# Kernel tuning notes

Hardware: AMD Instinct MI355X
Metric: run time of the kernel (lower is better)

Reference implementation:

```python
import jax, jax.numpy as jnp
import numpy as np

WS = 7          # window size
SHIFT = 3       # shift size for mask pattern
HP = WP = 224   # padded feature-map size -> (224/7)^2 = 1024 windows
DIM = 128
HEADS = 4
BATCH_IMGS = 8


def _rel_pos_index(ws: int) -> np.ndarray:
    coords = np.stack(np.meshgrid(np.arange(ws), np.arange(ws), indexing='ij'))  # [2,ws,ws]
    cf = coords.reshape(2, -1)                              # [2, ws*ws]
    rel = cf[:, :, None] - cf[:, None, :]                   # [2, N, N]
    rel = rel.transpose(1, 2, 0).copy()                     # [N, N, 2]
    rel[:, :, 0] += ws - 1
    rel[:, :, 1] += ws - 1
    rel[:, :, 0] *= 2 * ws - 1
    return rel.sum(-1).astype(np.int32)                     # [N, N]


def _shift_mask(Hp: int, Wp: int, ws: int, shift: int) -> np.ndarray:
    img = np.zeros((Hp, Wp), dtype=np.float32)
    slices = (slice(0, -ws), slice(-ws, -shift), slice(-shift, None))
    cnt = 0
    for hs in slices:
        for wsl in slices:
            img[hs, wsl] = cnt
            cnt += 1
    # window partition -> [nW, ws*ws]
    mw = img.reshape(Hp // ws, ws, Wp // ws, ws).transpose(0, 2, 1, 3).reshape(-1, ws * ws)
    am = mw[:, None, :] - mw[:, :, None]                    # [nW, N, N]
    return np.where(am != 0, np.float32(-100.0), np.float32(0.0))


def setup_inputs() -> dict:
    key = jax.random.key(0)
    ks = jax.random.split(key, 6)
    nW = (HP // WS) * (WP // WS)                            # 1024
    B_ = BATCH_IMGS * nW                                    # 8192
    N = WS * WS                                             # 49
    x = jax.random.normal(ks[0], (B_, N, DIM), dtype=jnp.float32)
    qkv_w = jax.random.normal(ks[1], (3 * DIM, DIM), dtype=jnp.float32) * (DIM ** -0.5)
    qkv_b = jax.random.normal(ks[2], (3 * DIM,), dtype=jnp.float32) * 0.02
    proj_w = jax.random.normal(ks[3], (DIM, DIM), dtype=jnp.float32) * (DIM ** -0.5)
    proj_b = jax.random.normal(ks[4], (DIM,), dtype=jnp.float32) * 0.02
    rpb_table = jax.random.normal(ks[5], ((2 * WS - 1) ** 2, HEADS), dtype=jnp.float32) * 0.02
    mask = jnp.asarray(_shift_mask(HP, WP, WS, SHIFT))      # [1024, 49, 49]
    rel_index = jnp.asarray(_rel_pos_index(WS))             # [49, 49] int32
    return {"x": x, "qkv_w": qkv_w, "qkv_b": qkv_b, "proj_w": proj_w,
            "proj_b": proj_b, "rpb_table": rpb_table, "mask": mask,
            "rel_index": rel_index}


def reference(x, qkv_w, qkv_b, proj_w, proj_b, rpb_table, mask, rel_index):
    B_, N, C = x.shape
    H = HEADS
    hd = C // H
    scale = hd ** -0.5
    qkv = x @ qkv_w.T + qkv_b                               # [B_, N, 3C]
    qkv = qkv.reshape(B_, N, 3, H, hd).transpose(2, 0, 3, 1, 4)  # [3, B_, H, N, hd]
    q, k, v = qkv[0], qkv[1], qkv[2]
    attn = jnp.einsum('bhnd,bhmd->bhnm', q * scale, k)      # [B_, H, N, N]
    # gathered relative position bias: table[(N*N)] -> [N, N, H] -> [H, N, N]
    bias = rpb_table[rel_index.reshape(-1)].reshape(N, N, H).transpose(2, 0, 1)
    attn = attn + bias[None]
    nW = mask.shape[0]
    attn = attn.reshape(B_ // nW, nW, H, N, N) + mask[None, :, None]
    attn = attn.reshape(B_, H, N, N)
    attn = jax.nn.softmax(attn, axis=-1)
    out = jnp.einsum('bhnm,bhmd->bhnd', attn, v)            # [B_, H, N, hd]
    out = out.transpose(0, 2, 1, 3).reshape(B_, N, C)
    return out @ proj_w.T + proj_b
```

## Files before the change

### kernel.cpp

```cpp
#include <hip/hip_runtime.h>

typedef __bf16 bf16;
typedef bf16 bf16x4 __attribute__((ext_vector_type(4)));
typedef bf16 bf16x8 __attribute__((ext_vector_type(8)));
typedef float f32x4 __attribute__((ext_vector_type(4)));

#define MFMA16(a, b, c) __builtin_amdgcn_mfma_f32_16x16x32_bf16((a), (b), (c), 0, 0, 0)

#define XS_OFF 0
#define QF_OFF 13328
#define PAF_OFF 0
#define KF_OFF 32768
#define VTF_OFF 49152
#define AO_OFF 32768
#define SMEM_BYTES 65536

__global__ void prep_kernel(const float* __restrict__ qkv_w, const float* __restrict__ proj_w,
                            const float* __restrict__ rpb, const int* __restrict__ rel,
                            bf16* __restrict__ wq, bf16* __restrict__ wp,
                            float* __restrict__ biasg) {
  int i = blockIdx.x * 256 + threadIdx.x;
  if (i < 49152) {
    wq[i] = (bf16)qkv_w[i];
  } else if (i < 65536) {
    wp[i - 49152] = (bf16)proj_w[i - 49152];
  } else if (i < 75140) {
    int t = i - 65536;
    int nm = t % 2401, h = t / 2401;
    biasg[t] = rpb[rel[nm] * 4 + h];
  }
}

__global__ void __launch_bounds__(256, 2)
swin_kernel(const float* __restrict__ x, const float* __restrict__ qkv_b,
            const float* __restrict__ proj_b, const float* __restrict__ maskp,
            const bf16* __restrict__ wq, const bf16* __restrict__ wp,
            const float* __restrict__ biasg, float* __restrict__ outp) {
  __shared__ __align__(16) unsigned char smem[SMEM_BYTES];
  bf16* xsL  = (bf16*)(smem + XS_OFF);
  bf16* qfL  = (bf16*)(smem + QF_OFF);
  bf16* pafL = (bf16*)(smem + PAF_OFF);
  bf16* kfL  = (bf16*)(smem + KF_OFF);
  bf16* vtfL = (bf16*)(smem + VTF_OFF);
  bf16* aoL  = (bf16*)(smem + AO_OFF);

  const int tid = threadIdx.x;
  const int bi = blockIdx.x;
  const int img = bi & 7;
  const int widx = bi >> 3;
  const int b = img * 1024 + widx;
  const int w = tid >> 6;
  const int l = tid & 63;
  const int lane16 = l & 15;
  const int grp = l >> 4;
  const float scale = 0.17677669529663687f;

  {
    const float4* xb = (const float4*)(x + (size_t)b * 6272);
#pragma unroll
    for (int it = 0; it < 7; ++it) {
      int i = tid + it * 256;
      if (i < 1568) {
        float4 v = xb[i];
        int e = i << 2, row = e >> 7, col = e & 127;
        bf16x4 bv;
        bv[0] = (bf16)v.x; bv[1] = (bf16)v.y; bv[2] = (bf16)v.z; bv[3] = (bf16)v.w;
        *(bf16x4*)(xsL + row * 136 + col) = bv;
      }
    }
    int region = tid >> 5;
    int off = (tid & 31) * 8;
    bf16x8 zz;
#pragma unroll
    for (int q = 0; q < 8; ++q) zz[q] = (bf16)0.f;
    *(bf16x8*)(vtfL + (region * 2 + 1) * 512 + 256 + off) = zz;
  }
  __syncthreads();

  {
    bf16x8 ax[4][4];
#pragma unroll
    for (int nt = 0; nt < 4; ++nt) {
      int rw = nt * 16 + lane16; if (rw > 48) rw = 48;
#pragma unroll
      for (int kb = 0; kb < 4; ++kb)
        ax[nt][kb] = *(const bf16x8*)(xsL + rw * 136 + kb * 32 + grp * 8);
    }
#pragma unroll
    for (int jj = 0; jj < 6; ++jj) {
      const int jb = w * 6 + jj;
      const int j = jb * 16 + lane16;
      bf16x8 bw[4];
#pragma unroll
      for (int kb = 0; kb < 4; ++kb)
        bw[kb] = *(const bf16x8*)(wq + j * 128 + kb * 32 + grp * 8);
      const float bj = qkv_b[j];
      const int part = jb >> 3;
      const int h = (jb >> 1) & 3;
      const int d0 = (jb & 1) * 16;
#pragma unroll
      for (int nt = 0; nt < 4; ++nt) {
        f32x4 acc = {0.f, 0.f, 0.f, 0.f};
#pragma unroll
        for (int kb = 0; kb < 4; ++kb) acc = MFMA16(ax[nt][kb], bw[kb], acc);
#pragma unroll
        for (int r = 0; r < 4; ++r) {
          const int nrow = nt * 16 + grp * 4 + r;
          if (nrow < 49) {
            float v = acc[r] + bj;
            const int d = d0 + lane16;
            if (part == 0) {
              v *= scale;
              qfL[(((h * 4 + nt) * 64) + (grp * 4 + r) + ((d >> 3) << 4)) * 8 + (d & 7)] = (bf16)v;
            } else if (part == 1) {
              kfL[(((h * 4 + nt) * 64) + (grp * 4 + r) + ((d >> 3) << 4)) * 8 + (d & 7)] = (bf16)v;
            } else {
              const int dt = d >> 4, kb2 = nrow >> 5;
              const int lp = (d & 15) + (((nrow >> 3) & 3) << 4);
              vtfL[((((h * 2 + dt) * 2 + kb2) * 64) + lp) * 8 + (nrow & 7)] = (bf16)v;
            }
          }
        }
      }
    }
  }
  __syncthreads();

  const int h = w;
  f32x4 S[4][4];
  {
    bf16x8 qa[4], ka[4];
#pragma unroll
    for (int t = 0; t < 4; ++t) {
      qa[t] = *(const bf16x8*)(qfL + ((h * 4 + t) * 64 + l) * 8);
      ka[t] = *(const bf16x8*)(kfL + ((h * 4 + t) * 64 + l) * 8);
    }
#pragma unroll
    for (int nt = 0; nt < 4; ++nt)
#pragma unroll
      for (int mt = 0; mt < 4; ++mt) {
        f32x4 zz = {0.f, 0.f, 0.f, 0.f};
        S[nt][mt] = MFMA16(qa[nt], ka[mt], zz);
      }
  }
  __syncthreads();

  float rinv[4][4];
  {
    const float* biash = biasg + h * 2401;
    const float* maskw = maskp + (size_t)widx * 2401;
#pragma unroll
    for (int nt = 0; nt < 4; ++nt) {
#pragma unroll
      for (int mt = 0; mt < 4; ++mt) {
        const int m = mt * 16 + lane16;
#pragma unroll
        for (int r = 0; r < 4; ++r) {
          const int n = nt * 16 + grp * 4 + r;
          float s = S[nt][mt][r];
          if (m < 49) {
            if (n < 49) s += biash[n * 49 + m] + maskw[n * 49 + m];
          } else {
            s = -1e30f;
          }
          S[nt][mt][r] = s;
        }
      }
#pragma unroll
      for (int r = 0; r < 4; ++r) {
        float mx = fmaxf(fmaxf(S[nt][0][r], S[nt][1][r]), fmaxf(S[nt][2][r], S[nt][3][r]));
        mx = fmaxf(mx, __shfl_xor(mx, 1));
        mx = fmaxf(mx, __shfl_xor(mx, 2));
        mx = fmaxf(mx, __shfl_xor(mx, 4));
        mx = fmaxf(mx, __shfl_xor(mx, 8));
        float sum = 0.f;
#pragma unroll
        for (int mt = 0; mt < 4; ++mt) {
          float p = __expf(S[nt][mt][r] - mx);
          S[nt][mt][r] = p;
          sum += p;
        }
        sum += __shfl_xor(sum, 1);
        sum += __shfl_xor(sum, 2);
        sum += __shfl_xor(sum, 4);
        sum += __shfl_xor(sum, 8);
        rinv[nt][r] = 1.f / sum;
      }
#pragma unroll
      for (int mt = 0; mt < 4; ++mt) {
        const int m = mt * 16 + lane16;
        const int kb2 = m >> 5;
        const int lpb = (grp * 4) + (((m >> 3) & 3) << 4);
#pragma unroll
        for (int r = 0; r < 4; ++r) {
          float p = (m < 49) ? S[nt][mt][r] : 0.f;
          pafL[((((w * 4 + nt) * 2 + kb2) * 64) + lpb + r) * 8 + (m & 7)] = (bf16)p;
        }
      }
    }
  }

  {
    bf16x8 vb2[2][2], pa[4][2];
#pragma unroll
    for (int dt = 0; dt < 2; ++dt)
#pragma unroll
      for (int kb = 0; kb < 2; ++kb)
        vb2[dt][kb] = *(const bf16x8*)(vtfL + (((h * 2 + dt) * 2 + kb) * 64 + l) * 8);
#pragma unroll
    for (int nt = 0; nt < 4; ++nt)
#pragma unroll
      for (int kb = 0; kb < 2; ++kb)
        pa[nt][kb] = *(const bf16x8*)(pafL + (((w * 4 + nt) * 2 + kb) * 64 + l) * 8);
    f32x4 O[4][2];
#pragma unroll
    for (int nt = 0; nt < 4; ++nt)
#pragma unroll
      for (int dt = 0; dt < 2; ++dt) {
        f32x4 acc = {0.f, 0.f, 0.f, 0.f};
        acc = MFMA16(pa[nt][0], vb2[dt][0], acc);
        acc = MFMA16(pa[nt][1], vb2[dt][1], acc);
        O[nt][dt] = acc;
      }
    __syncthreads();
#pragma unroll
    for (int nt = 0; nt < 4; ++nt)
#pragma unroll
      for (int r = 0; r < 4; ++r) {
        const int n = nt * 16 + grp * 4 + r;
        if (n < 49) {
          const float ri = rinv[nt][r];
#pragma unroll
          for (int dt = 0; dt < 2; ++dt) {
            const int c = h * 32 + dt * 16 + lane16;
            aoL[n * 136 + c] = (bf16)(O[nt][dt][r] * ri);
          }
        }
      }
  }
  __syncthreads();

  {
    bf16x8 aa[4][4];
#pragma unroll
    for (int nt = 0; nt < 4; ++nt) {
      int rw = nt * 16 + lane16; if (rw > 48) rw = 48;
#pragma unroll
      for (int kb = 0; kb < 4; ++kb)
        aa[nt][kb] = *(const bf16x8*)(aoL + rw * 136 + kb * 32 + grp * 8);
    }
    float* outb = outp + (size_t)b * 6272;
#pragma unroll
    for (int ee = 0; ee < 2; ++ee) {
      const int eb = w * 2 + ee;
      const int e = eb * 16 + lane16;
      bf16x8 bw[4];
#pragma unroll
      for (int kb = 0; kb < 4; ++kb)
        bw[kb] = *(const bf16x8*)(wp + e * 128 + kb * 32 + grp * 8);
      const float be = proj_b[e];
#pragma unroll
      for (int nt = 0; nt < 4; ++nt) {
        f32x4 acc = {0.f, 0.f, 0.f, 0.f};
#pragma unroll
        for (int kb = 0; kb < 4; ++kb) acc = MFMA16(aa[nt][kb], bw[kb], acc);
#pragma unroll
        for (int r = 0; r < 4; ++r) {
          const int n = nt * 16 + grp * 4 + r;
          if (n < 49) outb[n * 128 + e] = acc[r] + be;
        }
      }
    }
  }
}

extern "C" void kernel_launch(void* const* d_in, const int* in_sizes, int n_in,
                              void* d_out, int out_size, void* d_ws, size_t ws_size,
                              hipStream_t stream) {
  const float* x      = (const float*)d_in[0];
  const float* qkv_w  = (const float*)d_in[1];
  const float* qkv_b  = (const float*)d_in[2];
  const float* proj_w = (const float*)d_in[3];
  const float* proj_b = (const float*)d_in[4];
  const float* rpb    = (const float*)d_in[5];
  const float* maskp  = (const float*)d_in[6];
  const int*   rel    = (const int*)d_in[7];

  bf16* wq = (bf16*)d_ws;
  bf16* wp = wq + 49152;
  float* biasg = (float*)((char*)d_ws + 131072);

  prep_kernel<<<294, 256, 0, stream>>>(qkv_w, proj_w, rpb, rel, wq, wp, biasg);
  swin_kernel<<<8192, 256, 0, stream>>>(x, qkv_b, proj_b, maskp, wq, wp, biasg,
                                        (float*)d_out);
}
```

Measured before the change: 635.3 us.

## Restructure Swin attention kernel: register-loaded x, row-major LDS layouts, padded bf16 mask

The x tile is now loaded from global memory straight into MFMA operand registers, which drops the LDS staging step and a barrier. Q, K and V^T move to padded row-major LDS layouts written with vector stores, using swapped MFMA operands. Softmax now runs row-wise in registers with vector loads of a 64x64 padded bias and a bf16 mask that the prep kernel builds on each call, and P is normalized before the PV product. LDS use drops so that three blocks fit per CU, and the output is written with float4 stores. In exchange, the prep kernel does more work per call converting the full mask, and the mask and P values are held in bf16.

```diff
diff --git a/kernel.cpp b/kernel.cpp
--- a/kernel.cpp
+++ b/kernel.cpp
@@ -7,42 +7,46 @@
 
 #define MFMA16(a, b, c) __builtin_amdgcn_mfma_f32_16x16x32_bf16((a), (b), (c), 0, 0, 0)
 
-#define XS_OFF 0
-#define QF_OFF 13328
-#define PAF_OFF 0
-#define KF_OFF 32768
-#define VTF_OFF 49152
-#define AO_OFF 32768
-#define SMEM_BYTES 65536
+#define VT_OFF 0
+#define Q_OFF 18432
+#define K_OFF 35840
+#define PN_OFF 18432
+#define AO_OFF 18432
+#define SMEM_BYTES 53248
 
 __global__ void prep_kernel(const float* __restrict__ qkv_w, const float* __restrict__ proj_w,
                             const float* __restrict__ rpb, const int* __restrict__ rel,
+                            const float* __restrict__ mask,
                             bf16* __restrict__ wq, bf16* __restrict__ wp,
-                            float* __restrict__ biasg) {
+                            float* __restrict__ biasp, bf16* __restrict__ maskb) {
   int i = blockIdx.x * 256 + threadIdx.x;
-  if (i < 49152) {
-    wq[i] = (bf16)qkv_w[i];
-  } else if (i < 65536) {
-    wp[i - 49152] = (bf16)proj_w[i - 49152];
-  } else if (i < 75140) {
-    int t = i - 65536;
-    int nm = t % 2401, h = t / 2401;
-    biasg[t] = rpb[rel[nm] * 4 + h];
+  if (i < 49152) { wq[i] = (bf16)qkv_w[i]; return; }
+  i -= 49152;
+  if (i < 16384) { wp[i] = (bf16)proj_w[i]; return; }
+  i -= 16384;
+  if (i < 16384) {
+    int h = i >> 12, n = (i >> 6) & 63, m = i & 63;
+    biasp[i] = (n < 49 && m < 49) ? rpb[rel[n * 49 + m] * 4 + h] : 0.f;
+    return;
+  }
+  i -= 16384;
+  if (i < 4194304) {
+    int wi = i >> 12, n = (i >> 6) & 63, m = i & 63;
+    maskb[i] = (bf16)((n < 49 && m < 49) ? mask[wi * 2401 + n * 49 + m] : 0.f);
   }
 }
 
-__global__ void __launch_bounds__(256, 2)
+__global__ void __launch_bounds__(256, 3)
 swin_kernel(const float* __restrict__ x, const float* __restrict__ qkv_b,
-            const float* __restrict__ proj_b, const float* __restrict__ maskp,
-            const bf16* __restrict__ wq, const bf16* __restrict__ wp,
-            const float* __restrict__ biasg, float* __restrict__ outp) {
+            const float* __restrict__ proj_b, const bf16* __restrict__ wq,
+            const bf16* __restrict__ wp, const float* __restrict__ biasp,
+            const bf16* __restrict__ maskb, float* __restrict__ outp) {
   __shared__ __align__(16) unsigned char smem[SMEM_BYTES];
-  bf16* xsL  = (bf16*)(smem + XS_OFF);
-  bf16* qfL  = (bf16*)(smem + QF_OFF);
-  bf16* pafL = (bf16*)(smem + PAF_OFF);
-  bf16* kfL  = (bf16*)(smem + KF_OFF);
-  bf16* vtfL = (bf16*)(smem + VTF_OFF);
-  bf16* aoL  = (bf16*)(smem + AO_OFF);
+  bf16* vtL = (bf16*)(smem + VT_OFF);
+  bf16* qL  = (bf16*)(smem + Q_OFF);
+  bf16* kL  = (bf16*)(smem + K_OFF);
+  bf16* pnL = (bf16*)(smem + PN_OFF);
+  bf16* aoL = (bf16*)(smem + AO_OFF);
 
   const int tid = threadIdx.x;
   const int bi = blockIdx.x;
@@ -51,76 +55,67 @@
   const int b = img * 1024 + widx;
   const int w = tid >> 6;
   const int l = tid & 63;
-  const int lane16 = l & 15;
+  const int l16 = l & 15;
   const int grp = l >> 4;
   const float scale = 0.17677669529663687f;
 
-  {
-    const float4* xb = (const float4*)(x + (size_t)b * 6272);
-#pragma unroll
-    for (int it = 0; it < 7; ++it) {
-      int i = tid + it * 256;
-      if (i < 1568) {
-        float4 v = xb[i];
-        int e = i << 2, row = e >> 7, col = e & 127;
-        bf16x4 bv;
-        bv[0] = (bf16)v.x; bv[1] = (bf16)v.y; bv[2] = (bf16)v.z; bv[3] = (bf16)v.w;
-        *(bf16x4*)(xsL + row * 136 + col) = bv;
-      }
-    }
-    int region = tid >> 5;
-    int off = (tid & 31) * 8;
-    bf16x8 zz;
-#pragma unroll
-    for (int q = 0; q < 8; ++q) zz[q] = (bf16)0.f;
-    *(bf16x8*)(vtfL + (region * 2 + 1) * 512 + 256 + off) = zz;
-  }
-  __syncthreads();
-
-  {
-    bf16x8 ax[4][4];
+  bf16x8 xf[4][4];
+  {
+    const float* xb = x + (size_t)b * 6272;
 #pragma unroll
     for (int nt = 0; nt < 4; ++nt) {
-      int rw = nt * 16 + lane16; if (rw > 48) rw = 48;
-#pragma unroll
-      for (int kb = 0; kb < 4; ++kb)
-        ax[nt][kb] = *(const bf16x8*)(xsL + rw * 136 + kb * 32 + grp * 8);
-    }
-#pragma unroll
-    for (int jj = 0; jj < 6; ++jj) {
-      const int jb = w * 6 + jj;
-      const int j = jb * 16 + lane16;
-      bf16x8 bw[4];
-#pragma unroll
-      for (int kb = 0; kb < 4; ++kb)
-        bw[kb] = *(const bf16x8*)(wq + j * 128 + kb * 32 + grp * 8);
-      const float bj = qkv_b[j];
-      const int part = jb >> 3;
-      const int h = (jb >> 1) & 3;
-      const int d0 = (jb & 1) * 16;
-#pragma unroll
-      for (int nt = 0; nt < 4; ++nt) {
-        f32x4 acc = {0.f, 0.f, 0.f, 0.f};
-#pragma unroll
-        for (int kb = 0; kb < 4; ++kb) acc = MFMA16(ax[nt][kb], bw[kb], acc);
+      int n = nt * 16 + l16; if (n > 48) n = 48;
+      const float* rp = xb + n * 128 + grp * 8;
+#pragma unroll
+      for (int kb = 0; kb < 4; ++kb) {
+        float4 lo = *(const float4*)(rp + kb * 32);
+        float4 hi = *(const float4*)(rp + kb * 32 + 4);
+        bf16x8 r;
+        r[0] = (bf16)lo.x; r[1] = (bf16)lo.y; r[2] = (bf16)lo.z; r[3] = (bf16)lo.w;
+        r[4] = (bf16)hi.x; r[5] = (bf16)hi.y; r[6] = (bf16)hi.z; r[7] = (bf16)hi.w;
+        xf[nt][kb] = r;
+      }
+    }
+  }
+#pragma unroll
+  for (int jj = 0; jj < 6; ++jj) {
+    const int jb = w * 6 + jj;
+    bf16x8 wf[4];
+    const bf16* wrow = wq + (jb * 16 + l16) * 128 + grp * 8;
+#pragma unroll
+    for (int kb = 0; kb < 4; ++kb) wf[kb] = *(const bf16x8*)(wrow + kb * 32);
+    if (jb < 16) {
+      float4 b4 = *(const float4*)(qkv_b + jb * 16 + (grp << 2));
+      const int col = ((jb & 7) << 4) + (grp << 2);
+      bf16* dst = (jb < 8) ? qL : kL;
+      const float sc = (jb < 8) ? scale : 1.f;
+#pragma unroll
+      for (int nt = 0; nt < 4; ++nt) {
+        f32x4 acc = {0.f, 0.f, 0.f, 0.f};
+#pragma unroll
+        for (int kb = 0; kb < 4; ++kb) acc = MFMA16(wf[kb], xf[nt][kb], acc);
+        bf16x4 pv;
+#pragma unroll
+        for (int r = 0; r < 4; ++r) pv[r] = (bf16)((acc[r] + b4[r]) * sc);
+        *(bf16x4*)(dst + (nt * 16 + l16) * 136 + col) = pv;
+      }
+    } else {
+      const float bj = qkv_b[jb * 16 + l16];
+      const int d = ((jb - 16) << 4) + l16;
+#pragma unroll
+      for (int nt = 0; nt < 4; ++nt) {
+        f32x4 acc = {0.f, 0.f, 0.f, 0.f};
+#pragma unroll
+        for (int kb = 0; kb < 4; ++kb) acc = MFMA16(xf[nt][kb], wf[kb], acc);
+        const int n0 = nt * 16 + (grp << 2);
+        bf16x4 pv;
 #pragma unroll
         for (int r = 0; r < 4; ++r) {
-          const int nrow = nt * 16 + grp * 4 + r;
-          if (nrow < 49) {
-            float v = acc[r] + bj;
-            const int d = d0 + lane16;
-            if (part == 0) {
-              v *= scale;
-              qfL[(((h * 4 + nt) * 64) + (grp * 4 + r) + ((d >> 3) << 4)) * 8 + (d & 7)] = (bf16)v;
-            } else if (part == 1) {
-              kfL[(((h * 4 + nt) * 64) + (grp * 4 + r) + ((d >> 3) << 4)) * 8 + (d & 7)] = (bf16)v;
-            } else {
-              const int dt = d >> 4, kb2 = nrow >> 5;
-              const int lp = (d & 15) + (((nrow >> 3) & 3) << 4);
-              vtfL[((((h * 2 + dt) * 2 + kb2) * 64) + lp) * 8 + (nrow & 7)] = (bf16)v;
-            }
-          }
-        }
+          float v = acc[r] + bj;
+          if (nt == 3) v = (n0 + r < 49) ? v : 0.f;
+          pv[r] = (bf16)v;
+        }
+        *(bf16x4*)(vtL + d * 72 + n0) = pv;
       }
     }
   }
@@ -132,142 +127,130 @@
     bf16x8 qa[4], ka[4];
 #pragma unroll
     for (int t = 0; t < 4; ++t) {
-      qa[t] = *(const bf16x8*)(qfL + ((h * 4 + t) * 64 + l) * 8);
-      ka[t] = *(const bf16x8*)(kfL + ((h * 4 + t) * 64 + l) * 8);
-    }
+      qa[t] = *(const bf16x8*)(qL + (t * 16 + l16) * 136 + h * 32 + grp * 8);
+      ka[t] = *(const bf16x8*)(kL + (t * 16 + l16) * 136 + h * 32 + grp * 8);
+    }
+#pragma unroll
+    for (int mt = 0; mt < 4; ++mt)
+#pragma unroll
+      for (int nt = 0; nt < 4; ++nt) {
+        f32x4 z = {0.f, 0.f, 0.f, 0.f};
+        S[mt][nt] = MFMA16(ka[mt], qa[nt], z);
+      }
+  }
+  __syncthreads();
+
+  {
+    const float* bh = biasp + h * 4096;
+    const bf16* mw = maskb + (size_t)widx * 4096;
+#pragma unroll
+    for (int nt = 0; nt < 4; ++nt) {
+      const int n = nt * 16 + l16;
+      const int rowo = n * 64 + (grp << 2);
+      float p[4][4];
+#pragma unroll
+      for (int mt = 0; mt < 4; ++mt) {
+        float4 b4 = *(const float4*)(bh + rowo + mt * 16);
+        bf16x4 m4 = *(const bf16x4*)(mw + rowo + mt * 16);
+#pragma unroll
+        for (int r = 0; r < 4; ++r) {
+          float s = S[mt][nt][r] + b4[r] + (float)m4[r];
+          if (mt == 3) s = ((grp << 2) + r < 1) ? s : -1e30f;
+          p[mt][r] = s;
+        }
+      }
+      float mx = p[0][0];
+#pragma unroll
+      for (int mt = 0; mt < 4; ++mt)
+#pragma unroll
+        for (int r = 0; r < 4; ++r) mx = fmaxf(mx, p[mt][r]);
+      mx = fmaxf(mx, __shfl_xor(mx, 16));
+      mx = fmaxf(mx, __shfl_xor(mx, 32));
+      float sum = 0.f;
+#pragma unroll
+      for (int mt = 0; mt < 4; ++mt)
+#pragma unroll
+        for (int r = 0; r < 4; ++r) { float e = __expf(p[mt][r] - mx); p[mt][r] = e; sum += e; }
+      sum += __shfl_xor(sum, 16);
+      sum += __shfl_xor(sum, 32);
+      const float ri = 1.f / sum;
+      if (n < 49) {
+        bf16* pd = pnL + h * 3528 + n * 72 + (grp << 2);
+#pragma unroll
+        for (int mt = 0; mt < 4; ++mt) {
+          bf16x4 pv;
+#pragma unroll
+          for (int r = 0; r < 4; ++r) pv[r] = (bf16)(p[mt][r] * ri);
+          *(bf16x4*)(pd + mt * 16) = pv;
+        }
+      }
+    }
+  }
+
+  f32x4 O[4][2];
+  {
+    bf16x8 pa[4][2], vb[2][2];
 #pragma unroll
     for (int nt = 0; nt < 4; ++nt)
 #pragma unroll
-      for (int mt = 0; mt < 4; ++mt) {
-        f32x4 zz = {0.f, 0.f, 0.f, 0.f};
-        S[nt][mt] = MFMA16(qa[nt], ka[mt], zz);
-      }
-  }
-  __syncthreads();
-
-  float rinv[4][4];
-  {
-    const float* biash = biasg + h * 2401;
-    const float* maskw = maskp + (size_t)widx * 2401;
-#pragma unroll
-    for (int nt = 0; nt < 4; ++nt) {
-#pragma unroll
-      for (int mt = 0; mt < 4; ++mt) {
-        const int m = mt * 16 + lane16;
-#pragma unroll
-        for (int r = 0; r < 4; ++r) {
-          const int n = nt * 16 + grp * 4 + r;
-          float s = S[nt][mt][r];
-          if (m < 49) {
-            if (n < 49) s += biash[n * 49 + m] + maskw[n * 49 + m];
-          } else {
-            s = -1e30f;
-          }
-          S[nt][mt][r] = s;
-        }
-      }
+      for (int kb = 0; kb < 2; ++kb)
+        pa[nt][kb] = *(const bf16x8*)(pnL + h * 3528 + (nt * 16 + l16) * 72 + kb * 32 + grp * 8);
+#pragma unroll
+    for (int dt = 0; dt < 2; ++dt)
+#pragma unroll
+      for (int kb = 0; kb < 2; ++kb)
+        vb[dt][kb] = *(const bf16x8*)(vtL + (h * 32 + dt * 16 + l16) * 72 + kb * 32 + grp * 8);
+#pragma unroll
+    for (int nt = 0; nt < 4; ++nt)
+#pragma unroll
+      for (int dt = 0; dt < 2; ++dt) {
+        f32x4 acc = {0.f, 0.f, 0.f, 0.f};
+        acc = MFMA16(pa[nt][0], vb[dt][0], acc);
+        acc = MFMA16(pa[nt][1], vb[dt][1], acc);
+        O[nt][dt] = acc;
+      }
+  }
+  __syncthreads();
+#pragma unroll
+  for (int nt = 0; nt < 4; ++nt)
+#pragma unroll
+    for (int dt = 0; dt < 2; ++dt) {
+      const int c = h * 32 + dt * 16 + l16;
 #pragma unroll
       for (int r = 0; r < 4; ++r) {
-        float mx = fmaxf(fmaxf(S[nt][0][r], S[nt][1][r]), fmaxf(S[nt][2][r], S[nt][3][r]));
-        mx = fmaxf(mx, __shfl_xor(mx, 1));
-        mx = fmaxf(mx, __shfl_xor(mx, 2));
-        mx = fmaxf(mx, __shfl_xor(mx, 4));
-        mx = fmaxf(mx, __shfl_xor(mx, 8));
-        float sum = 0.f;
-#pragma unroll
-        for (int mt = 0; mt < 4; ++mt) {
-          float p = __expf(S[nt][mt][r] - mx);
-          S[nt][mt][r] = p;
-          sum += p;
-        }
-        sum += __shfl_xor(sum, 1);
-        sum += __shfl_xor(sum, 2);
-        sum += __shfl_xor(sum, 4);
-        sum += __shfl_xor(sum, 8);
-        rinv[nt][r] = 1.f / sum;
-      }
-#pragma unroll
-      for (int mt = 0; mt < 4; ++mt) {
-        const int m = mt * 16 + lane16;
-        const int kb2 = m >> 5;
-        const int lpb = (grp * 4) + (((m >> 3) & 3) << 4);
-#pragma unroll
-        for (int r = 0; r < 4; ++r) {
-          float p = (m < 49) ? S[nt][mt][r] : 0.f;
-          pafL[((((w * 4 + nt) * 2 + kb2) * 64) + lpb + r) * 8 + (m & 7)] = (bf16)p;
-        }
-      }
-    }
-  }
-
-  {
-    bf16x8 vb2[2][2], pa[4][2];
-#pragma unroll
-    for (int dt = 0; dt < 2; ++dt)
-#pragma unroll
-      for (int kb = 0; kb < 2; ++kb)
-        vb2[dt][kb] = *(const bf16x8*)(vtfL + (((h * 2 + dt) * 2 + kb) * 64 + l) * 8);
+        const int n = nt * 16 + (grp << 2) + r;
+        aoL[n * 136 + c] = (bf16)O[nt][dt][r];
+      }
+    }
+  __syncthreads();
+
+  {
+    bf16x8 af[4][4];
 #pragma unroll
     for (int nt = 0; nt < 4; ++nt)
 #pragma unroll
-      for (int kb = 0; kb < 2; ++kb)
-        pa[nt][kb] = *(const bf16x8*)(pafL + (((w * 4 + nt) * 2 + kb) * 64 + l) * 8);
-    f32x4 O[4][2];
-#pragma unroll
-    for (int nt = 0; nt < 4; ++nt)
-#pragma unroll
-      for (int dt = 0; dt < 2; ++dt) {
-        f32x4 acc = {0.f, 0.f, 0.f, 0.f};
-        acc = MFMA16(pa[nt][0], vb2[dt][0], acc);
-        acc = MFMA16(pa[nt][1], vb2[dt][1], acc);
-        O[nt][dt] = acc;
-      }
-    __syncthreads();
-#pragma unroll
-    for (int nt = 0; nt < 4; ++nt)
-#pragma unroll
-      for (int r = 0; r < 4; ++r) {
-        const int n = nt * 16 + grp * 4 + r;
-        if (n < 49) {
-          const float ri = rinv[nt][r];
-#pragma unroll
-          for (int dt = 0; dt < 2; ++dt) {
-            const int c = h * 32 + dt * 16 + lane16;
-            aoL[n * 136 + c] = (bf16)(O[nt][dt][r] * ri);
-          }
-        }
-      }
-  }
-  __syncthreads();
-
-  {
-    bf16x8 aa[4][4];
-#pragma unroll
-    for (int nt = 0; nt < 4; ++nt) {
-      int rw = nt * 16 + lane16; if (rw > 48) rw = 48;
-#pragma unroll
       for (int kb = 0; kb < 4; ++kb)
-        aa[nt][kb] = *(const bf16x8*)(aoL + rw * 136 + kb * 32 + grp * 8);
-    }
-    float* outb = outp + (size_t)b * 6272;
+        af[nt][kb] = *(const bf16x8*)(aoL + (nt * 16 + l16) * 136 + kb * 32 + grp * 8);
+    float* ob = outp + (size_t)b * 6272;
 #pragma unroll
     for (int ee = 0; ee < 2; ++ee) {
       const int eb = w * 2 + ee;
-      const int e = eb * 16 + lane16;
-      bf16x8 bw[4];
-#pragma unroll
-      for (int kb = 0; kb < 4; ++kb)
-        bw[kb] = *(const bf16x8*)(wp + e * 128 + kb * 32 + grp * 8);
-      const float be = proj_b[e];
-#pragma unroll
-      for (int nt = 0; nt < 4; ++nt) {
-        f32x4 acc = {0.f, 0.f, 0.f, 0.f};
-#pragma unroll
-        for (int kb = 0; kb < 4; ++kb) acc = MFMA16(aa[nt][kb], bw[kb], acc);
-#pragma unroll
-        for (int r = 0; r < 4; ++r) {
-          const int n = nt * 16 + grp * 4 + r;
-          if (n < 49) outb[n * 128 + e] = acc[r] + be;
+      bf16x8 wa[4];
+      const bf16* wrow = wp + (eb * 16 + l16) * 128 + grp * 8;
+#pragma unroll
+      for (int kb = 0; kb < 4; ++kb) wa[kb] = *(const bf16x8*)(wrow + kb * 32);
+      float4 pb4 = *(const float4*)(proj_b + eb * 16 + (grp << 2));
+#pragma unroll
+      for (int nt = 0; nt < 4; ++nt) {
+        f32x4 acc = {0.f, 0.f, 0.f, 0.f};
+#pragma unroll
+        for (int kb = 0; kb < 4; ++kb) acc = MFMA16(wa[kb], af[nt][kb], acc);
+        const int n = nt * 16 + l16;
+        if (n < 49) {
+          float4 o4;
+          o4.x = acc[0] + pb4.x; o4.y = acc[1] + pb4.y;
+          o4.z = acc[2] + pb4.z; o4.w = acc[3] + pb4.w;
+          *(float4*)(ob + n * 128 + eb * 16 + (grp << 2)) = o4;
         }
       }
     }
@@ -286,11 +269,13 @@
   const float* maskp  = (const float*)d_in[6];
   const int*   rel    = (const int*)d_in[7];
 
-  bf16* wq = (bf16*)d_ws;
-  bf16* wp = wq + 49152;
-  float* biasg = (float*)((char*)d_ws + 131072);
-
-  prep_kernel<<<294, 256, 0, stream>>>(qkv_w, proj_w, rpb, rel, wq, wp, biasg);
-  swin_kernel<<<8192, 256, 0, stream>>>(x, qkv_b, proj_b, maskp, wq, wp, biasg,
+  bf16* wq     = (bf16*)d_ws;
+  bf16* wp     = (bf16*)((char*)d_ws + 98304);
+  float* biasp = (float*)((char*)d_ws + 131072);
+  bf16* maskb  = (bf16*)((char*)d_ws + 196608);
+
+  prep_kernel<<<16704, 256, 0, stream>>>(qkv_w, proj_w, rpb, rel, maskp,
+                                         wq, wp, biasp, maskb);
+  swin_kernel<<<8192, 256, 0, stream>>>(x, qkv_b, proj_b, wq, wp, biasp, maskb,
                                         (float*)d_out);
 }
```

Result: faster. 620.0 us (-2.4%).
